# Optimization experiments

Measured on AMD Instinct MI355X. Metric: run time of the kernel, lower is better.

Reference implementation:

```python
import jax, jax.numpy as jnp
import numpy as np

B = 2
C = 1024
H = 16
D = C // H  # 64
L_S, L_T, L_C = 2048, 1024, 512
MODS = ["shape", "texture", "color"]
SCALE_RMS = np.sqrt(D).astype(np.float32)
SCALE_ATTN = 1.0 / np.sqrt(D).astype(np.float32)


def _rms(x, gamma):
    # F.normalize(x, dim=-1) * gamma * sqrt(dim); x: [B,L,H,D], gamma: [H,D]
    n = jnp.linalg.norm(x, axis=-1, keepdims=True)
    return x / jnp.maximum(n, 1e-12) * gamma * SCALE_RMS


def _sdpa(q, k, v):
    # q: [B,Lq,H,D], k/v: [B,Lk,H,D] -> [B,Lq,H,D]
    s = jnp.einsum("blhd,bmhd->bhlm", q, k) * SCALE_ATTN
    a = jax.nn.softmax(s, axis=-1)
    return jnp.einsum("bhlm,bmhd->blhd", a, v)


def setup_inputs() -> dict:
    key = jax.random.key(0)
    ks = jax.random.split(key, 32)
    inp = {}
    lens = {"shape": L_S, "texture": L_T, "color": L_C}
    i = 0
    for m in MODS:
        inp[f"x_{m}"] = jax.random.normal(ks[i], (B, lens[m], C), jnp.float32); i += 1
        inp[f"Wqkv_{m}"] = jax.random.normal(ks[i], (C, 3 * C), jnp.float32) * 0.02; i += 1
        inp[f"bqkv_{m}"] = jnp.zeros((3 * C,), jnp.float32)
        inp[f"gq_{m}"] = jnp.ones((H, D), jnp.float32)
        inp[f"gk_{m}"] = jnp.ones((H, D), jnp.float32)
        inp[f"Wout_{m}"] = jax.random.normal(ks[i], (C, C), jnp.float32) * 0.02; i += 1
        inp[f"bout_{m}"] = jnp.zeros((C,), jnp.float32)
    return inp


def _forward(x_shape, x_texture, x_color,
             Wqkv_shape, bqkv_shape, gq_shape, gk_shape, Wout_shape, bout_shape,
             Wqkv_texture, bqkv_texture, gq_texture, gk_texture, Wout_texture, bout_texture,
             Wqkv_color, bqkv_color, gq_color, gk_color, Wout_color, bout_color):
    xs = {"shape": x_shape, "texture": x_texture, "color": x_color}
    Wqkv = {"shape": Wqkv_shape, "texture": Wqkv_texture, "color": Wqkv_color}
    bqkv = {"shape": bqkv_shape, "texture": bqkv_texture, "color": bqkv_color}
    gq = {"shape": gq_shape, "texture": gq_texture, "color": gq_color}
    gk = {"shape": gk_shape, "texture": gk_texture, "color": gk_color}
    Wout = {"shape": Wout_shape, "texture": Wout_texture, "color": Wout_color}
    bout = {"shape": bout_shape, "texture": bout_texture, "color": bout_color}

    q, k, v = {}, {}, {}
    for m in MODS:
        L = xs[m].shape[1]
        qkv = (xs[m] @ Wqkv[m] + bqkv[m]).reshape(B, L, 3, H, D)
        _q, _k, _v = qkv[:, :, 0], qkv[:, :, 1], qkv[:, :, 2]
        q[m] = _rms(_q, gq[m])
        k[m] = _rms(_k, gk[m])
        v[m] = _v

    # protected modality attends only to itself
    h = {"shape": _sdpa(q["shape"], k["shape"], v["shape"])}

    # other modalities: joint attention over [others ; detached protected]
    others = ["texture", "color"]
    q_o = jnp.concatenate([q[m] for m in others], axis=1)
    k_all = jnp.concatenate([k[m] for m in others] + [jax.lax.stop_gradient(k["shape"])], axis=1)
    v_all = jnp.concatenate([v[m] for m in others] + [jax.lax.stop_gradient(v["shape"])], axis=1)
    h_o = _sdpa(q_o, k_all, v_all)
    h["texture"] = h_o[:, :L_T]
    h["color"] = h_o[:, L_T:L_T + L_C]

    outs = []
    for m in MODS:
        L = h[m].shape[1]
        outs.append(h[m].reshape(B, L, C) @ Wout[m] + bout[m])
    return tuple(outs)


def reference(x_shape, x_texture, x_color,
              Wqkv_shape, bqkv_shape, gq_shape, gk_shape, Wout_shape, bout_shape,
              Wqkv_texture, bqkv_texture, gq_texture, gk_texture, Wout_texture, bout_texture,
              Wqkv_color, bqkv_color, gq_color, gk_color, Wout_color, bout_color):
    return _forward(x_shape, x_texture, x_color,
                    Wqkv_shape, bqkv_shape, gq_shape, gk_shape, Wout_shape, bout_shape,
                    Wqkv_texture, bqkv_texture, gq_texture, gk_texture, Wout_texture, bout_texture,
                    Wqkv_color, bqkv_color, gq_color, gk_color, Wout_color, bout_color)
```

## Files before the change

kernel.cpp:

```cpp
#include <hip/hip_runtime.h>
#include <hip/hip_bf16.h>
#include <stdint.h>

typedef unsigned short u16;
typedef unsigned int u32;
typedef __attribute__((ext_vector_type(8))) short bf16x8;
typedef __attribute__((ext_vector_type(4))) float f32x4;
typedef __attribute__((ext_vector_type(2))) unsigned int u32x2;
typedef __attribute__((ext_vector_type(4))) unsigned short u16x4;
typedef __attribute__((ext_vector_type(8))) unsigned short u16x8;

#define DEV __device__ __forceinline__

DEV u16 f2bf(float f){
  unsigned u = __float_as_uint(f);
  return (u16)((u + 0x7FFFu + ((u >> 16) & 1u)) >> 16);
}
DEV float b2f(u16 v){ return __uint_as_float(((unsigned)v) << 16); }

DEV u32 cvtpk(float lo, float hi){
  u32 r;
  asm("v_cvt_pk_bf16_f32 %0, %1, %2" : "=v"(r) : "v"(lo), "v"(hi));
  return r;
}

DEV f32x4 MFMA(bf16x8 a, bf16x8 b, f32x4 c){
  return __builtin_amdgcn_mfma_f32_16x16x32_bf16(a, b, c, 0, 0, 0);
}

DEV void gload16(const u16* g, u16* l){
  __builtin_amdgcn_global_load_lds((const __attribute__((address_space(1))) u32*)g,
                                   (__attribute__((address_space(3))) u32*)l, 16, 0, 0);
}

__global__ __launch_bounds__(256) void cvt_f32_bf16(const float* __restrict__ in,
                                                    u16* __restrict__ out, int n4){
  int i = blockIdx.x * 256 + threadIdx.x;
  if (i >= n4) return;
  f32x4 v = ((const f32x4*)in)[i];
  u16x4 o;
  o[0] = f2bf(v[0]); o[1] = f2bf(v[1]); o[2] = f2bf(v[2]); o[3] = f2bf(v[3]);
  ((u16x4*)out)[i] = o;
}

__global__ __launch_bounds__(256) void tcvt(const float* __restrict__ in, u16* __restrict__ out,
                                            int R, int C){
  __shared__ float tile[64][65];
  int c0 = blockIdx.x * 64, r0 = blockIdx.y * 64;
  int t = threadIdx.x;
#pragma unroll
  for (int j = 0; j < 16; j++){
    int idx = j * 256 + t;
    int r = idx >> 6, c = idx & 63;
    tile[r][c] = in[(size_t)(r0 + r) * C + c0 + c];
  }
  __syncthreads();
#pragma unroll
  for (int j = 0; j < 16; j++){
    int idx = j * 256 + t;
    int c = idx >> 6, r = idx & 63;
    out[(size_t)(c0 + c) * R + r0 + r] = f2bf(tile[r][c]);
  }
}

template<int F32OUT>
__global__ __launch_bounds__(256) void gemm3(const u16* __restrict__ A0, const u16* __restrict__ A1,
                                             const u16* __restrict__ A2,
                                             const u16* __restrict__ B0, const u16* __restrict__ B1,
                                             const u16* __restrict__ B2,
                                             const float* __restrict__ bi0, const float* __restrict__ bi1,
                                             const float* __restrict__ bi2,
                                             void* __restrict__ o0, void* __restrict__ o1,
                                             void* __restrict__ o2,
                                             int N, int K, int rb0, int rb1){
  __shared__ __align__(16) u16 smA[128 * 32];
  __shared__ __align__(16) u16 smB[128 * 32];
  int yb = blockIdx.y;
  const u16 *A, *Bt; const float* bias; void* outp;
  int m0;
  if (yb < rb0)            { A = A0; Bt = B0; bias = bi0; outp = o0; m0 = yb * 128; }
  else if (yb < rb0 + rb1) { A = A1; Bt = B1; bias = bi1; outp = o1; m0 = (yb - rb0) * 128; }
  else                     { A = A2; Bt = B2; bias = bi2; outp = o2; m0 = (yb - rb0 - rb1) * 128; }

  int t = threadIdx.x;
  int lane = t & 63, w = t >> 6;
  int wr = w >> 1, wc = w & 1;
  int li = lane & 15, g = lane >> 4;
  int n0 = blockIdx.x * 128;

  int srow = w * 32 + (lane >> 2);
  int sk = (lane & 3) * 8;
  const u16* Ag0 = A  + (size_t)(m0 + srow) * K + sk;
  const u16* Ag1 = A  + (size_t)(m0 + srow + 16) * K + sk;
  const u16* Bg0 = Bt + (size_t)(n0 + srow) * K + sk;
  const u16* Bg1 = Bt + (size_t)(n0 + srow + 16) * K + sk;
  u16* la0 = &smA[w * 1024];
  u16* la1 = &smA[w * 1024 + 512];
  u16* lb0 = &smB[w * 1024];
  u16* lb1 = &smB[w * 1024 + 512];

  f32x4 acc[4][4] = {};

  for (int kt = 0; kt < K; kt += 32){
    __syncthreads();
    gload16(Ag0 + kt, la0);
    gload16(Ag1 + kt, la1);
    gload16(Bg0 + kt, lb0);
    gload16(Bg1 + kt, lb1);
    __syncthreads();

    bf16x8 af[4], bfr[4];
#pragma unroll
    for (int mf = 0; mf < 4; mf++)
      af[mf] = *(const bf16x8*)&smA[(wr * 64 + mf * 16 + li) * 32 + g * 8];
#pragma unroll
    for (int nf = 0; nf < 4; nf++)
      bfr[nf] = *(const bf16x8*)&smB[(wc * 64 + nf * 16 + li) * 32 + g * 8];
#pragma unroll
    for (int mf = 0; mf < 4; mf++)
#pragma unroll
      for (int nf = 0; nf < 4; nf++)
        acc[mf][nf] = MFMA(af[mf], bfr[nf], acc[mf][nf]);
  }

#pragma unroll
  for (int mf = 0; mf < 4; mf++){
    int row = m0 + wr * 64 + mf * 16 + g * 4;
#pragma unroll
    for (int nf = 0; nf < 4; nf++){
      int col = n0 + wc * 64 + nf * 16 + li;
      float bs = bias[col];
#pragma unroll
      for (int r = 0; r < 4; r++){
        float v = acc[mf][nf][r] + bs;
        if (F32OUT) ((float*)outp)[(size_t)(row + r) * N + col] = v;
        else        ((u16*)outp)[(size_t)(row + r) * N + col]  = f2bf(v);
      }
    }
  }
}

__global__ __launch_bounds__(256) void rms_scatter(const u16* __restrict__ qkvb, int L,
                                                   const float* __restrict__ gq, const float* __restrict__ gk,
                                                   u16* __restrict__ qdst, int qL, int qoff,
                                                   u16* __restrict__ kdst, int kvoff){
  int tok = blockIdx.x;
  int b = tok / L, l = tok - b * L;
  int t = threadIdx.x;
  int c = t * 4;
  int h = t >> 4;
  int d = c & 63;
  const u16* rowq = qkvb + (size_t)tok * 3072 + c;
  u16x4 qv = *(const u16x4*)rowq;
  u16x4 kv = *(const u16x4*)(rowq + 1024);
  float qf[4], kf[4], ssq = 0.f, ssk = 0.f;
#pragma unroll
  for (int j = 0; j < 4; j++){
    qf[j] = b2f(qv[j]); kf[j] = b2f(kv[j]);
    ssq += qf[j] * qf[j]; ssk += kf[j] * kf[j];
  }
#pragma unroll
  for (int msk = 1; msk < 16; msk <<= 1){
    ssq += __shfl_xor(ssq, msk);
    ssk += __shfl_xor(ssk, msk);
  }
  float sq = 1.44269504088896340736f / fmaxf(sqrtf(ssq), 1e-12f);
  float sk = 8.0f / fmaxf(sqrtf(ssk), 1e-12f);
  u16x4 qo, ko;
#pragma unroll
  for (int j = 0; j < 4; j++){
    qo[j] = f2bf(qf[j] * sq * gq[h * 64 + d + j]);
    ko[j] = f2bf(kf[j] * sk * gk[h * 64 + d + j]);
  }
  *(u16x4*)(qdst + ((size_t)(b * 16 + h) * qL + qoff + l) * 64 + d) = qo;
  *(u16x4*)(kdst + ((size_t)(b * 16 + h) * 3584 + kvoff + l) * 64 + d) = ko;
}

__global__ __launch_bounds__(256) void vtrans(const u16* __restrict__ qkvb, int L,
                                              u16* __restrict__ vT, int kvoff){
  __shared__ u16 tile[64][65];
  int l0 = blockIdx.x * 64; int h = blockIdx.y; int b = blockIdx.z;
  int t = threadIdx.x;
#pragma unroll
  for (int j = 0; j < 16; j++){
    int idx = j * 256 + t;
    int r = idx >> 6, d = idx & 63;
    tile[r][d] = qkvb[(size_t)(b * L + l0 + r) * 3072 + 2048 + h * 64 + d];
  }
  __syncthreads();
#pragma unroll
  for (int j = 0; j < 16; j++){
    int idx = j * 256 + t;
    int d = idx >> 6, r = idx & 63;
    vT[((size_t)(b * 16 + h) * 64 + d) * 3584 + kvoff + l0 + r] = tile[r][d];
  }
}

__global__ __launch_bounds__(128, 3) void attn(const u16* __restrict__ q0, const u16* __restrict__ q1,
                                               const u16* __restrict__ kmat, const u16* __restrict__ vTm,
                                               u16* __restrict__ ob0, u16* __restrict__ ob1,
                                               u16* __restrict__ ob2){
  __shared__ __align__(16) u16 smK[64 * 72];
  __shared__ __align__(16) u16 smV[64 * 72];
  __shared__ __align__(16) u16 smP[2][32 * 68];
  int lin = blockIdx.x;
  bool t1 = lin < 768;
  int rel = t1 ? lin : lin - 768;
  int qb = rel >> 5, hb = rel & 31;
  int h = hb & 15, b = hb >> 4;
  int bh = b * 16 + h;
  const u16* qp = t1 ? q1 : q0;
  int Lq  = t1 ? 1536 : 2048;
  int kvo = t1 ? 0    : 1536;
  int Lk  = t1 ? 3584 : 2048;
  u16* out0 = t1 ? ob1 : ob0;  int L0 = t1 ? 1024 : 2048;
  u16* out1 = t1 ? ob2 : ob0;  int L1 = t1 ? 512  : 2048;

  int t = threadIdx.x, lane = t & 63, w = t >> 6;
  int li = lane & 15, g = lane >> 4;

  const u16* qbase = qp + ((size_t)bh * Lq + qb * 64 + w * 32) * 64;
  bf16x8 qa[2][2];
#pragma unroll
  for (int qg = 0; qg < 2; qg++)
#pragma unroll
    for (int kh = 0; kh < 2; kh++)
      qa[qg][kh] = *(const bf16x8*)(qbase + (size_t)(qg * 16 + li) * 64 + kh * 32 + g * 8);

  f32x4 acc[2][4] = {};
  float mrunL[2] = {-3.0e38f, -3.0e38f};
  float lsumL[2] = {0.f, 0.f};

  const u16* kbase = kmat + ((size_t)bh * 3584 + kvo) * 64;
  const u16* vbase = vTm + (size_t)bh * 64 * 3584 + kvo;
  u16* pp = &smP[w][0];

  u16x8 ka[4], va[4];
#pragma unroll
  for (int j = 0; j < 4; j++){
    int u = t + j * 128; int ur = u >> 3, us = (u & 7) * 8;
    ka[j] = *(const u16x8*)(kbase + (size_t)ur * 64 + us);
    va[j] = *(const u16x8*)(vbase + (size_t)ur * 3584 + us);
  }

  for (int kt = 0; kt < Lk; kt += 64){
    __syncthreads();
#pragma unroll
    for (int j = 0; j < 4; j++){
      int u = t + j * 128; int ur = u >> 3, us = (u & 7) * 8;
      *(u16x8*)&smK[ur * 72 + us] = ka[j];
      *(u16x8*)&smV[ur * 72 + us] = va[j];
    }
    __syncthreads();
    if (kt + 64 < Lk){
#pragma unroll
      for (int j = 0; j < 4; j++){
        int u = t + j * 128; int ur = u >> 3, us = (u & 7) * 8;
        ka[j] = *(const u16x8*)(kbase + (size_t)(kt + 64 + ur) * 64 + us);
        va[j] = *(const u16x8*)(vbase + (size_t)ur * 3584 + kt + 64 + us);
      }
    }

    f32x4 sT[2][4];
    __builtin_amdgcn_s_setprio(1);
#pragma unroll
    for (int kg = 0; kg < 4; kg++){
      bf16x8 kf0 = *(const bf16x8*)&smK[(kg * 16 + li) * 72 + g * 8];
      bf16x8 kf1 = *(const bf16x8*)&smK[(kg * 16 + li) * 72 + 32 + g * 8];
#pragma unroll
      for (int qg = 0; qg < 2; qg++){
        f32x4 z = {};
        z = MFMA(kf0, qa[qg][0], z);
        sT[qg][kg] = MFMA(kf1, qa[qg][1], z);
      }
    }
    __builtin_amdgcn_s_setprio(0);

    float rm[2];
#pragma unroll
    for (int qg = 0; qg < 2; qg++){
      float m01 = fmaxf(fmaxf(sT[qg][0][0], sT[qg][0][1]), fmaxf(sT[qg][0][2], sT[qg][0][3]));
      float m23 = fmaxf(fmaxf(sT[qg][1][0], sT[qg][1][1]), fmaxf(sT[qg][1][2], sT[qg][1][3]));
      float m45 = fmaxf(fmaxf(sT[qg][2][0], sT[qg][2][1]), fmaxf(sT[qg][2][2], sT[qg][2][3]));
      float m67 = fmaxf(fmaxf(sT[qg][3][0], sT[qg][3][1]), fmaxf(sT[qg][3][2], sT[qg][3][3]));
      float v = fmaxf(fmaxf(m01, m23), fmaxf(m45, m67));
      v = fmaxf(v, __shfl_xor(v, 16));
      v = fmaxf(v, __shfl_xor(v, 32));
      rm[qg] = v;
    }

    if (__any((rm[0] > mrunL[0]) | (rm[1] > mrunL[1]))){
#pragma unroll
      for (int qg = 0; qg < 2; qg++){
        float mo = mrunL[qg];
        float mn = fmaxf(mo, rm[qg]);
        float al = __builtin_exp2f(mo - mn);
        mrunL[qg] = mn;
        lsumL[qg] *= al;
#pragma unroll
        for (int dt = 0; dt < 4; dt++)
#pragma unroll
          for (int r = 0; r < 4; r++) acc[qg][dt][r] *= al;
      }
    }

#pragma unroll
    for (int qg = 0; qg < 2; qg++){
      float mn = mrunL[qg];
      float ps = 0.f;
#pragma unroll
      for (int kg = 0; kg < 4; kg++){
        float p0 = __builtin_exp2f(sT[qg][kg][0] - mn);
        float p1 = __builtin_exp2f(sT[qg][kg][1] - mn);
        float p2 = __builtin_exp2f(sT[qg][kg][2] - mn);
        float p3 = __builtin_exp2f(sT[qg][kg][3] - mn);
        ps += (p0 + p1) + (p2 + p3);
        u32x2 pk; pk[0] = cvtpk(p0, p1); pk[1] = cvtpk(p2, p3);
        *(u32x2*)&pp[(qg * 16 + li) * 68 + kg * 16 + g * 4] = pk;
      }
      lsumL[qg] += ps;
    }

    bf16x8 pf[2][2];
#pragma unroll
    for (int qg = 0; qg < 2; qg++){
      pf[qg][0] = *(const bf16x8*)&pp[(qg * 16 + li) * 68 + g * 8];
      pf[qg][1] = *(const bf16x8*)&pp[(qg * 16 + li) * 68 + 32 + g * 8];
    }
    __builtin_amdgcn_s_setprio(1);
#pragma unroll
    for (int dt = 0; dt < 4; dt++){
      bf16x8 vf0 = *(const bf16x8*)&smV[(dt * 16 + li) * 72 + g * 8];
      bf16x8 vf1 = *(const bf16x8*)&smV[(dt * 16 + li) * 72 + 32 + g * 8];
#pragma unroll
      for (int qg = 0; qg < 2; qg++){
        acc[qg][dt] = MFMA(vf0, pf[qg][0], acc[qg][dt]);
        acc[qg][dt] = MFMA(vf1, pf[qg][1], acc[qg][dt]);
      }
    }
    __builtin_amdgcn_s_setprio(0);
  }

#pragma unroll
  for (int qg = 0; qg < 2; qg++){
    float ls = lsumL[qg];
    ls += __shfl_xor(ls, 16);
    ls += __shfl_xor(ls, 32);
    float inv = 1.0f / ls;
    int qi = qb * 64 + w * 32 + qg * 16 + li;
    u16* dst; size_t basei;
    if (qi < L0){ dst = out0; basei = ((size_t)(b * L0 + qi)) * 1024 + h * 64; }
    else        { dst = out1; basei = ((size_t)(b * L1 + (qi - L0))) * 1024 + h * 64; }
#pragma unroll
    for (int dt = 0; dt < 4; dt++){
      u16x4 o;
#pragma unroll
      for (int r = 0; r < 4; r++) o[r] = f2bf(acc[qg][dt][r] * inv);
      *(u16x4*)&dst[basei + dt * 16 + g * 4] = o;
    }
  }
}

extern "C" void kernel_launch(void* const* d_in, const int* in_sizes, int n_in,
                              void* d_out, int out_size, void* d_ws, size_t ws_size,
                              hipStream_t stream){
  (void)in_sizes; (void)n_in; (void)out_size; (void)ws_size;
  const float* x[3]    = {(const float*)d_in[0],  (const float*)d_in[7],  (const float*)d_in[14]};
  const float* Wqkv[3] = {(const float*)d_in[1],  (const float*)d_in[8],  (const float*)d_in[15]};
  const float* bqkv[3] = {(const float*)d_in[2],  (const float*)d_in[9],  (const float*)d_in[16]};
  const float* gq[3]   = {(const float*)d_in[3],  (const float*)d_in[10], (const float*)d_in[17]};
  const float* gk[3]   = {(const float*)d_in[4],  (const float*)d_in[11], (const float*)d_in[18]};
  const float* Wout[3] = {(const float*)d_in[5],  (const float*)d_in[12], (const float*)d_in[19]};
  const float* bout[3] = {(const float*)d_in[6],  (const float*)d_in[13], (const float*)d_in[20]};
  float* outp = (float*)d_out;

  const int Ms[3] = {4096, 2048, 1024};
  const int Ls[3] = {2048, 1024, 512};
  const int kvoffs[3] = {1536, 0, 1024};

  u16* base = (u16*)d_ws;
  size_t off = 0;
  auto nxt = [&](size_t e){ u16* r = base + off; off += e; return r; };
  u16* xbf[3];  for (int m = 0; m < 3; m++) xbf[m]  = nxt((size_t)Ms[m] * 1024);
  u16* WqT[3];  for (int m = 0; m < 3; m++) WqT[m]  = nxt((size_t)3072 * 1024);
  u16* WoT[3];  for (int m = 0; m < 3; m++) WoT[m]  = nxt((size_t)1024 * 1024);
  u16* qkvb[3]; for (int m = 0; m < 3; m++) qkvb[m] = nxt((size_t)Ms[m] * 3072);
  u16* qA = nxt((size_t)2 * 16 * 2048 * 64);
  u16* qB = nxt((size_t)2 * 16 * 1536 * 64);
  u16* kB = nxt((size_t)2 * 16 * 3584 * 64);
  u16* vT = WqT[0];
  u16* hb[3]; for (int m = 0; m < 3; m++) hb[m] = xbf[m];

  for (int m = 0; m < 3; m++){
    int n4 = Ms[m] * 1024 / 4;
    cvt_f32_bf16<<<n4 / 256, 256, 0, stream>>>(x[m], xbf[m], n4);
    tcvt<<<dim3(3072 / 64, 1024 / 64), 256, 0, stream>>>(Wqkv[m], WqT[m], 1024, 3072);
    tcvt<<<dim3(1024 / 64, 1024 / 64), 256, 0, stream>>>(Wout[m], WoT[m], 1024, 1024);
  }
  gemm3<0><<<dim3(3072 / 128, 56), 256, 0, stream>>>(
      xbf[0], xbf[1], xbf[2], WqT[0], WqT[1], WqT[2],
      bqkv[0], bqkv[1], bqkv[2], qkvb[0], qkvb[1], qkvb[2],
      3072, 1024, 32, 16);
  rms_scatter<<<Ms[0], 256, 0, stream>>>(qkvb[0], Ls[0], gq[0], gk[0], qA, 2048, 0,    kB, 1536);
  rms_scatter<<<Ms[1], 256, 0, stream>>>(qkvb[1], Ls[1], gq[1], gk[1], qB, 1536, 0,    kB, 0);
  rms_scatter<<<Ms[2], 256, 0, stream>>>(qkvb[2], Ls[2], gq[2], gk[2], qB, 1536, 1024, kB, 1024);
  for (int m = 0; m < 3; m++)
    vtrans<<<dim3(Ls[m] / 64, 16, 2), 256, 0, stream>>>(qkvb[m], Ls[m], vT, kvoffs[m]);
  attn<<<1792, 128, 0, stream>>>(qA, qB, kB, vT, hb[0], hb[1], hb[2]);
  float* outs[3] = {outp, outp + (size_t)4096 * 1024, outp + (size_t)6144 * 1024};
  gemm3<1><<<dim3(1024 / 128, 56), 256, 0, stream>>>(
      hb[0], hb[1], hb[2], WoT[0], WoT[1], WoT[2],
      bout[0], bout[1], bout[2], outs[0], outs[1], outs[2],
      1024, 1024, 32, 16);
}
```

Before: 500.3 us.

## Double-buffer GEMM LDS tiles and merge per-modality prep kernels into single launches

The GEMM now keeps two LDS buffers and issues the next k-tile's global-to-LDS loads before computing on the current one. That removes one barrier per iteration and overlaps load latency with MFMA work. The per-modality conversion, transpose, RMS-norm scatter and V-transpose launches are each merged into one kernel that picks its modality from the block index, cutting the launch count from about 17 to 6. The prefetch relies on a single barrier per iteration and on the async LDS loads completing before the next read, which adds a correctness risk and doubles GEMM LDS use.

```diff
diff --git a/kernel.cpp b/kernel.cpp
--- a/kernel.cpp
+++ b/kernel.cpp
@@ -33,20 +33,42 @@
                                    (__attribute__((address_space(3))) u32*)l, 16, 0, 0);
 }
 
-__global__ __launch_bounds__(256) void cvt_f32_bf16(const float* __restrict__ in,
-                                                    u16* __restrict__ out, int n4){
+__global__ __launch_bounds__(256) void cvt3(const float* __restrict__ x0, const float* __restrict__ x1,
+                                            const float* __restrict__ x2, u16* __restrict__ out){
   int i = blockIdx.x * 256 + threadIdx.x;
-  if (i >= n4) return;
-  f32x4 v = ((const f32x4*)in)[i];
+  const float* src; int base;
+  if (i < 1048576)      { src = x0; base = 0; }
+  else if (i < 1572864) { src = x1; base = 1048576; }
+  else                  { src = x2; base = 1572864; }
+  f32x4 v = ((const f32x4*)src)[i - base];
   u16x4 o;
   o[0] = f2bf(v[0]); o[1] = f2bf(v[1]); o[2] = f2bf(v[2]); o[3] = f2bf(v[3]);
   ((u16x4*)out)[i] = o;
 }
 
-__global__ __launch_bounds__(256) void tcvt(const float* __restrict__ in, u16* __restrict__ out,
-                                            int R, int C){
+__global__ __launch_bounds__(256) void tcvt6(const float* __restrict__ q0, const float* __restrict__ q1,
+                                             const float* __restrict__ q2,
+                                             const float* __restrict__ o0, const float* __restrict__ o1,
+                                             const float* __restrict__ o2,
+                                             u16* __restrict__ Q0, u16* __restrict__ Q1, u16* __restrict__ Q2,
+                                             u16* __restrict__ O0, u16* __restrict__ O1, u16* __restrict__ O2){
   __shared__ float tile[64][65];
-  int c0 = blockIdx.x * 64, r0 = blockIdx.y * 64;
+  int lin = blockIdx.x;
+  const float* in; u16* out; int C, u;
+  if (lin < 2304){
+    int s = lin / 768; u = lin - s * 768;
+    in = s == 0 ? q0 : (s == 1 ? q1 : q2);
+    out = s == 0 ? Q0 : (s == 1 ? Q1 : Q2);
+    C = 3072;
+  } else {
+    int s = (lin - 2304) / 256; u = (lin - 2304) - s * 256;
+    in = s == 0 ? o0 : (s == 1 ? o1 : o2);
+    out = s == 0 ? O0 : (s == 1 ? O1 : O2);
+    C = 1024;
+  }
+  int ct = C >> 6;
+  int c0 = (u % ct) * 64, r0 = (u / ct) * 64;
+  const int R = 1024;
   int t = threadIdx.x;
 #pragma unroll
   for (int j = 0; j < 16; j++){
@@ -73,8 +95,8 @@
                                              void* __restrict__ o0, void* __restrict__ o1,
                                              void* __restrict__ o2,
                                              int N, int K, int rb0, int rb1){
-  __shared__ __align__(16) u16 smA[128 * 32];
-  __shared__ __align__(16) u16 smB[128 * 32];
+  __shared__ __align__(16) u16 smA[2][128 * 32];
+  __shared__ __align__(16) u16 smB[2][128 * 32];
   int yb = blockIdx.y;
   const u16 *A, *Bt; const float* bias; void* outp;
   int m0;
@@ -94,33 +116,37 @@
   const u16* Ag1 = A  + (size_t)(m0 + srow + 16) * K + sk;
   const u16* Bg0 = Bt + (size_t)(n0 + srow) * K + sk;
   const u16* Bg1 = Bt + (size_t)(n0 + srow + 16) * K + sk;
-  u16* la0 = &smA[w * 1024];
-  u16* la1 = &smA[w * 1024 + 512];
-  u16* lb0 = &smB[w * 1024];
-  u16* lb1 = &smB[w * 1024 + 512];
+  int wb = w * 1024;
+
+  gload16(Ag0, &smA[0][wb]);
+  gload16(Ag1, &smA[0][wb + 512]);
+  gload16(Bg0, &smB[0][wb]);
+  gload16(Bg1, &smB[0][wb + 512]);
 
   f32x4 acc[4][4] = {};
-
+  int cur = 0;
   for (int kt = 0; kt < K; kt += 32){
     __syncthreads();
-    gload16(Ag0 + kt, la0);
-    gload16(Ag1 + kt, la1);
-    gload16(Bg0 + kt, lb0);
-    gload16(Bg1 + kt, lb1);
-    __syncthreads();
-
+    if (kt + 32 < K){
+      int nx = cur ^ 1;
+      gload16(Ag0 + kt + 32, &smA[nx][wb]);
+      gload16(Ag1 + kt + 32, &smA[nx][wb + 512]);
+      gload16(Bg0 + kt + 32, &smB[nx][wb]);
+      gload16(Bg1 + kt + 32, &smB[nx][wb + 512]);
+    }
     bf16x8 af[4], bfr[4];
 #pragma unroll
     for (int mf = 0; mf < 4; mf++)
-      af[mf] = *(const bf16x8*)&smA[(wr * 64 + mf * 16 + li) * 32 + g * 8];
+      af[mf] = *(const bf16x8*)&smA[cur][(wr * 64 + mf * 16 + li) * 32 + g * 8];
 #pragma unroll
     for (int nf = 0; nf < 4; nf++)
-      bfr[nf] = *(const bf16x8*)&smB[(wc * 64 + nf * 16 + li) * 32 + g * 8];
+      bfr[nf] = *(const bf16x8*)&smB[cur][(wc * 64 + nf * 16 + li) * 32 + g * 8];
 #pragma unroll
     for (int mf = 0; mf < 4; mf++)
 #pragma unroll
       for (int nf = 0; nf < 4; nf++)
         acc[mf][nf] = MFMA(af[mf], bfr[nf], acc[mf][nf]);
+    cur ^= 1;
   }
 
 #pragma unroll
@@ -140,17 +166,25 @@
   }
 }
 
-__global__ __launch_bounds__(256) void rms_scatter(const u16* __restrict__ qkvb, int L,
-                                                   const float* __restrict__ gq, const float* __restrict__ gk,
-                                                   u16* __restrict__ qdst, int qL, int qoff,
-                                                   u16* __restrict__ kdst, int kvoff){
+__global__ __launch_bounds__(256) void rms3(const u16* __restrict__ qkvb0, const u16* __restrict__ qkvb1,
+                                            const u16* __restrict__ qkvb2,
+                                            const float* __restrict__ gq0, const float* __restrict__ gk0,
+                                            const float* __restrict__ gq1, const float* __restrict__ gk1,
+                                            const float* __restrict__ gq2, const float* __restrict__ gk2,
+                                            u16* __restrict__ qA, u16* __restrict__ qB,
+                                            u16* __restrict__ kB){
   int tok = blockIdx.x;
-  int b = tok / L, l = tok - b * L;
+  const u16* qkvb; const float *gq, *gk; u16* qdst;
+  int L, qL, qoff, kvoff, rel;
+  if (tok < 4096)      { rel = tok;        qkvb = qkvb0; gq = gq0; gk = gk0; qdst = qA; L = 2048; qL = 2048; qoff = 0;    kvoff = 1536; }
+  else if (tok < 6144) { rel = tok - 4096; qkvb = qkvb1; gq = gq1; gk = gk1; qdst = qB; L = 1024; qL = 1536; qoff = 0;    kvoff = 0; }
+  else                 { rel = tok - 6144; qkvb = qkvb2; gq = gq2; gk = gk2; qdst = qB; L = 512;  qL = 1536; qoff = 1024; kvoff = 1024; }
+  int b = rel / L, l = rel - b * L;
   int t = threadIdx.x;
   int c = t * 4;
   int h = t >> 4;
   int d = c & 63;
-  const u16* rowq = qkvb + (size_t)tok * 3072 + c;
+  const u16* rowq = qkvb + (size_t)rel * 3072 + c;
   u16x4 qv = *(const u16x4*)rowq;
   u16x4 kv = *(const u16x4*)(rowq + 1024);
   float qf[4], kf[4], ssq = 0.f, ssk = 0.f;
@@ -173,13 +207,18 @@
     ko[j] = f2bf(kf[j] * sk * gk[h * 64 + d + j]);
   }
   *(u16x4*)(qdst + ((size_t)(b * 16 + h) * qL + qoff + l) * 64 + d) = qo;
-  *(u16x4*)(kdst + ((size_t)(b * 16 + h) * 3584 + kvoff + l) * 64 + d) = ko;
-}
-
-__global__ __launch_bounds__(256) void vtrans(const u16* __restrict__ qkvb, int L,
-                                              u16* __restrict__ vT, int kvoff){
+  *(u16x4*)(kB + ((size_t)(b * 16 + h) * 3584 + kvoff + l) * 64 + d) = ko;
+}
+
+__global__ __launch_bounds__(256) void vtrans3(const u16* __restrict__ qkvb0, const u16* __restrict__ qkvb1,
+                                               const u16* __restrict__ qkvb2, u16* __restrict__ vT){
   __shared__ u16 tile[64][65];
-  int l0 = blockIdx.x * 64; int h = blockIdx.y; int b = blockIdx.z;
+  int lt = blockIdx.x;
+  int h = blockIdx.y, b = blockIdx.z;
+  const u16* qkvb; int L, l0, kvoff;
+  if (lt < 32)      { qkvb = qkvb0; L = 2048; l0 = lt * 64;        kvoff = 1536; }
+  else if (lt < 48) { qkvb = qkvb1; L = 1024; l0 = (lt - 32) * 64; kvoff = 0; }
+  else              { qkvb = qkvb2; L = 512;  l0 = (lt - 48) * 64; kvoff = 1024; }
   int t = threadIdx.x;
 #pragma unroll
   for (int j = 0; j < 16; j++){
@@ -375,8 +414,6 @@
   float* outp = (float*)d_out;
 
   const int Ms[3] = {4096, 2048, 1024};
-  const int Ls[3] = {2048, 1024, 512};
-  const int kvoffs[3] = {1536, 0, 1024};
 
   u16* base = (u16*)d_ws;
   size_t off = 0;
@@ -391,21 +428,17 @@
   u16* vT = WqT[0];
   u16* hb[3]; for (int m = 0; m < 3; m++) hb[m] = xbf[m];
 
-  for (int m = 0; m < 3; m++){
-    int n4 = Ms[m] * 1024 / 4;
-    cvt_f32_bf16<<<n4 / 256, 256, 0, stream>>>(x[m], xbf[m], n4);
-    tcvt<<<dim3(3072 / 64, 1024 / 64), 256, 0, stream>>>(Wqkv[m], WqT[m], 1024, 3072);
-    tcvt<<<dim3(1024 / 64, 1024 / 64), 256, 0, stream>>>(Wout[m], WoT[m], 1024, 1024);
-  }
+  cvt3<<<7168, 256, 0, stream>>>(x[0], x[1], x[2], xbf[0]);
+  tcvt6<<<3072, 256, 0, stream>>>(Wqkv[0], Wqkv[1], Wqkv[2], Wout[0], Wout[1], Wout[2],
+                                  WqT[0], WqT[1], WqT[2], WoT[0], WoT[1], WoT[2]);
   gemm3<0><<<dim3(3072 / 128, 56), 256, 0, stream>>>(
       xbf[0], xbf[1], xbf[2], WqT[0], WqT[1], WqT[2],
       bqkv[0], bqkv[1], bqkv[2], qkvb[0], qkvb[1], qkvb[2],
       3072, 1024, 32, 16);
-  rms_scatter<<<Ms[0], 256, 0, stream>>>(qkvb[0], Ls[0], gq[0], gk[0], qA, 2048, 0,    kB, 1536);
-  rms_scatter<<<Ms[1], 256, 0, stream>>>(qkvb[1], Ls[1], gq[1], gk[1], qB, 1536, 0,    kB, 0);
-  rms_scatter<<<Ms[2], 256, 0, stream>>>(qkvb[2], Ls[2], gq[2], gk[2], qB, 1536, 1024, kB, 1024);
-  for (int m = 0; m < 3; m++)
-    vtrans<<<dim3(Ls[m] / 64, 16, 2), 256, 0, stream>>>(qkvb[m], Ls[m], vT, kvoffs[m]);
+  rms3<<<7168, 256, 0, stream>>>(qkvb[0], qkvb[1], qkvb[2],
+                                 gq[0], gk[0], gq[1], gk[1], gq[2], gk[2],
+                                 qA, qB, kB);
+  vtrans3<<<dim3(56, 16, 2), 256, 0, stream>>>(qkvb[0], qkvb[1], qkvb[2], vT);
   attn<<<1792, 128, 0, stream>>>(qA, qB, kB, vT, hb[0], hb[1], hb[2]);
   float* outs[3] = {outp, outp + (size_t)4096 * 1024, outp + (size_t)6144 * 1024};
   gemm3<1><<<dim3(1024 / 128, 56), 256, 0, stream>>>(
```

New measurement: 471.4 us. -5.8%, faster.
